# Kernel tuning notes

Hardware: AMD Instinct MI355X
Metric: run time of the kernel (lower is better)

Reference implementation:

```python
import math
import jax, jax.numpy as jnp
import numpy as np

DIM = 1024
NUM_HEADS = 16
HEAD_DIM = DIM // NUM_HEADS


def setup_inputs() -> dict:
    key = jax.random.key(0)
    ks = jax.random.split(key, 5)
    b, t, d = 2, 2048, DIM
    x = jax.random.normal(ks[0], (b, t, d), dtype=jnp.float32)
    mask = jnp.ones((b, t), dtype=jnp.float32)  # 1 = keep, 0 = pad
    s_in = 1.0 / math.sqrt(d)
    w_qkv = jax.random.normal(ks[1], (3 * d, d), dtype=jnp.float32) * s_in
    b_qkv = jnp.zeros((3 * d,), dtype=jnp.float32)
    w_out = jax.random.normal(ks[2], (d, d), dtype=jnp.float32) * s_in
    b_out = jnp.zeros((d,), dtype=jnp.float32)
    return {"x": x, "mask": mask, "w_qkv": w_qkv, "b_qkv": b_qkv,
            "w_out": w_out, "b_out": b_out}


def reference(x, mask, w_qkv, b_qkv, w_out, b_out):
    b, t, d = x.shape
    h, hd = NUM_HEADS, HEAD_DIM
    # qkv projection (torch Linear: x @ W^T + b)
    qkv = x @ w_qkv.T + b_qkv                          # [b,t,3d]
    q, k, v = jnp.split(qkv, 3, axis=-1)
    def reshape(z):
        return z.reshape(b, t, h, hd).transpose(0, 2, 1, 3)  # [b,h,t,hd]
    q, k, v = reshape(q), reshape(k), reshape(v)
    att = jnp.einsum('bhqd,bhkd->bhqk', q, k) / math.sqrt(hd)  # [b,h,t,t]
    causal = jnp.tril(jnp.ones((t, t), dtype=bool))            # [t,t]
    keep = causal[None, None, :, :] & (mask[:, None, None, :] != 0)
    att = jnp.where(keep, att, -jnp.inf)
    att = jax.nn.softmax(att, axis=-1)
    out = jnp.einsum('bhqk,bhkd->bhqd', att, v)        # [b,h,t,hd]
    out = out.transpose(0, 2, 1, 3).reshape(b, t, d)
    return out @ w_out.T + b_out
```

## Files before the change

kernel.cpp:

```cpp
#include <hip/hip_runtime.h>
#include <cmath>

#define B_ 2
#define T_ 2048
#define D_ 1024
#define H_ 16
#define HD_ 64
#define M_ (B_ * T_)
#define N3_ (3 * D_)
#define K_ 1024

typedef _Float16 halfx8 __attribute__((ext_vector_type(8)));
typedef _Float16 halfx4 __attribute__((ext_vector_type(4)));
typedef _Float16 halfx2 __attribute__((ext_vector_type(2)));
typedef __fp16 fp16x2 __attribute__((ext_vector_type(2)));
typedef float f32x4 __attribute__((ext_vector_type(4)));
typedef float f32x16 __attribute__((ext_vector_type(16)));

#define ASYNC_COPY16(gp, lp) \
  __builtin_amdgcn_global_load_lds((__attribute__((address_space(1))) void*)(gp), \
      (__attribute__((address_space(3))) void*)(lp), 16, 0, 0)

#define QSCALE 0.1803368801111204f
#define RTHR 4.0f

__device__ __forceinline__ float exp2fast(float x) {
#if __has_builtin(__builtin_amdgcn_exp2f)
    return __builtin_amdgcn_exp2f(x);
#else
    return exp2f(x);
#endif
}

__device__ const int QT2_OF[24] = {15,15,7, 14,14, 13,13,6, 12,12, 11,11,5, 10,10, 9,9,4, 8,8, 3,2,1,0};
__device__ const int C2_OF[24]  = { 0, 1,0,  0, 1,  0, 1,0,  0, 1,  0, 1,0,  0, 1, 0,1,0,  0,1, 0,0,0,0};

__global__ __launch_bounds__(256) void prep_all(
    const float* __restrict__ x, const float* __restrict__ wq,
    const float* __restrict__ wo, const float* __restrict__ mask,
    _Float16* __restrict__ xh, _Float16* __restrict__ wqh,
    _Float16* __restrict__ woh, float* __restrict__ kbias,
    int* __restrict__ tflags)
{
    int bid = blockIdx.x;
    if (bid >= 4096) {
        int i = (bid - 4096) * 256 + threadIdx.x;
        float mv = mask[i];
        kbias[i] = (mv != 0.f) ? 0.f : -INFINITY;
        unsigned long long bal = __ballot(mv != 0.f);
        if ((threadIdx.x & 63) == 0) tflags[i >> 6] = (bal == ~0ULL) ? 1 : 0;
        return;
    }
    const float* s; _Float16* d; int off;
    if (bid < 2048)      { s = x;  d = xh;  off = bid; }
    else if (bid < 3584) { s = wq; d = wqh; off = bid - 2048; }
    else                 { s = wo; d = woh; off = bid - 3584; }
    int i = (off * 256 + threadIdx.x) * 8;
    float4 a = *(const float4*)(s + i);
    float4 b = *(const float4*)(s + i + 4);
    halfx8 h;
    h[0] = (_Float16)a.x; h[1] = (_Float16)a.y; h[2] = (_Float16)a.z; h[3] = (_Float16)a.w;
    h[4] = (_Float16)b.x; h[5] = (_Float16)b.y; h[6] = (_Float16)b.z; h[7] = (_Float16)b.w;
    *(halfx8*)(d + i) = h;
}

__global__ __launch_bounds__(256) void gemm_qkv(
    const _Float16* __restrict__ A, const _Float16* __restrict__ Wt,
    const float* __restrict__ bias,
    _Float16* __restrict__ qh, _Float16* __restrict__ kh, _Float16* __restrict__ vth)
{
    __shared__ _Float16 As[128 * 32];
    __shared__ _Float16 Bs[128 * 32];
    const int tid = threadIdx.x;
    const int lane = tid & 63, w = tid >> 6;
    const int col = lane & 15, quad = lane >> 4;
    const int wr = w >> 1, wc = w & 1;
    const int m0 = blockIdx.y << 7, n0 = blockIdx.x << 7;

    const int c0 = w * 2, c1 = c0 + 1;
    const int r0 = c0 * 16 + (lane >> 2), r1 = c1 * 16 + (lane >> 2);
    const int ks = (lane & 3) << 3;

    f32x4 acc[4][4] = {};

    for (int k0 = 0; k0 < K_; k0 += 32) {
        ASYNC_COPY16(A  + (size_t)(m0 + r0) * K_ + k0 + ks, &As[c0 * 512]);
        ASYNC_COPY16(A  + (size_t)(m0 + r1) * K_ + k0 + ks, &As[c1 * 512]);
        ASYNC_COPY16(Wt + (size_t)(n0 + r0) * K_ + k0 + ks, &Bs[c0 * 512]);
        ASYNC_COPY16(Wt + (size_t)(n0 + r1) * K_ + k0 + ks, &Bs[c1 * 512]);
        __syncthreads();
        halfx8 af[4], bf[4];
#pragma unroll
        for (int i = 0; i < 4; ++i)
            af[i] = *(const halfx8*)&As[(wr * 64 + i * 16 + col) * 32 + quad * 8];
#pragma unroll
        for (int j = 0; j < 4; ++j)
            bf[j] = *(const halfx8*)&Bs[(wc * 64 + j * 16 + col) * 32 + quad * 8];
#pragma unroll
        for (int i = 0; i < 4; ++i)
#pragma unroll
            for (int j = 0; j < 4; ++j)
                acc[i][j] = __builtin_amdgcn_mfma_f32_16x16x32_f16(af[i], bf[j], acc[i][j], 0, 0, 0);
        __syncthreads();
    }

#pragma unroll
    for (int i = 0; i < 4; ++i) {
#pragma unroll
        for (int r = 0; r < 4; ++r) {
            int m = m0 + wr * 64 + i * 16 + quad * 4 + r;
            int bb = m >> 11, tt = m & (T_ - 1);
#pragma unroll
            for (int j = 0; j < 4; ++j) {
                int n = n0 + wc * 64 + j * 16 + col;
                float val = acc[i][j][r] + bias[n];
                int which = n >> 10, head = (n >> 6) & 15, dd = n & 63;
                if (which == 0) {
                    qh[((size_t)(bb * H_ + head) * T_ + tt) * HD_ + dd] = (_Float16)(val * QSCALE);
                } else if (which == 1) {
                    int hi = ((dd >> 3) ^ (tt & 7) ^ ((tt >> 3) & 7)) & 7;
                    int dds = (hi << 3) | (dd & 7);
                    kh[((size_t)(bb * H_ + head) * T_ + tt) * HD_ + dds] = (_Float16)val;
                } else {
                    int hi = (((tt >> 3) & 7) ^ (dd & 7) ^ ((dd >> 3) & 7)) & 7;
                    int tts = (tt & ~63) | (hi << 3) | (tt & 7);
                    vth[((size_t)(bb * H_ + head) * HD_ + dd) * T_ + tts] = (_Float16)val;
                }
            }
        }
    }
}

__global__ __launch_bounds__(256) void gemm_out(
    const _Float16* __restrict__ A, const _Float16* __restrict__ Wt,
    const float* __restrict__ bias, float* __restrict__ C)
{
    __shared__ _Float16 As[128 * 32];
    __shared__ _Float16 Bs[64 * 32];
    const int tid = threadIdx.x;
    const int lane = tid & 63, w = tid >> 6;
    const int col = lane & 15, quad = lane >> 4;
    const int m0 = blockIdx.y << 7, n0 = blockIdx.x << 6;

    const int c0 = w * 2, c1 = c0 + 1;
    const int rA0 = c0 * 16 + (lane >> 2), rA1 = c1 * 16 + (lane >> 2);
    const int rB = w * 16 + (lane >> 2);
    const int ks = (lane & 3) << 3;

    f32x4 acc[2][4] = {};

    for (int k0 = 0; k0 < K_; k0 += 32) {
        ASYNC_COPY16(A  + (size_t)(m0 + rA0) * K_ + k0 + ks, &As[c0 * 512]);
        ASYNC_COPY16(A  + (size_t)(m0 + rA1) * K_ + k0 + ks, &As[c1 * 512]);
        ASYNC_COPY16(Wt + (size_t)(n0 + rB) * K_ + k0 + ks, &Bs[w * 512]);
        __syncthreads();
        halfx8 af[2], bf[4];
#pragma unroll
        for (int i = 0; i < 2; ++i)
            af[i] = *(const halfx8*)&As[(w * 32 + i * 16 + col) * 32 + quad * 8];
#pragma unroll
        for (int j = 0; j < 4; ++j)
            bf[j] = *(const halfx8*)&Bs[(j * 16 + col) * 32 + quad * 8];
#pragma unroll
        for (int i = 0; i < 2; ++i)
#pragma unroll
            for (int j = 0; j < 4; ++j)
                acc[i][j] = __builtin_amdgcn_mfma_f32_16x16x32_f16(af[i], bf[j], acc[i][j], 0, 0, 0);
        __syncthreads();
    }

#pragma unroll
    for (int i = 0; i < 2; ++i) {
#pragma unroll
        for (int r = 0; r < 4; ++r) {
            int m = m0 + w * 32 + i * 16 + quad * 4 + r;
#pragma unroll
            for (int j = 0; j < 4; ++j) {
                int n = n0 + j * 16 + col;
                C[(size_t)m * D_ + n] = acc[i][j][r] + bias[n];
            }
        }
    }
}

__global__ __launch_bounds__(256, 3) void attn_kernel(
    const _Float16* __restrict__ qh, const _Float16* __restrict__ kh,
    const _Float16* __restrict__ vth, const float* __restrict__ kbias,
    const int* __restrict__ tflags,
    float* __restrict__ pm, float* __restrict__ pl,
    _Float16* __restrict__ po, _Float16* __restrict__ oh)
{
    __shared__ _Float16 Ks[2][64 * 64];
    __shared__ _Float16 Vt[2][64 * 64];

    const int item = blockIdx.x >> 5;
    const int qt = QT2_OF[item], c = C2_OF[item];
    const int hb = blockIdx.x & 31;
    const int h = hb & 15, b = hb >> 4;
    const bool split = (qt >= 8);
    const int tid = threadIdx.x;
    const int lane = tid & 63, w = tid >> 6;
    const int l31 = lane & 31, q2 = lane >> 5;

    const int kt0 = (split && c) ? (qt + 1) : 0;
    const int ktend = (split && !c) ? qt : (2 * qt + 1);

    const int bh = b * H_ + h;
    const _Float16* qp = qh + (size_t)bh * T_ * HD_;
    const _Float16* kp = kh + (size_t)bh * T_ * HD_;
    const _Float16* vp = vth + (size_t)bh * HD_ * T_;
    const float* kb = kbias + (size_t)b * T_;
    const int* tf = tflags + b * 32;

    const int qbase = qt * 128 + w * 32;
    const int q_row = qbase + l31;

    halfx8 bq[4];
#pragma unroll
    for (int hc = 0; hc < 4; ++hc)
        bq[hc] = *(const halfx8*)(qp + (size_t)q_row * HD_ + hc * 16 + q2 * 8);

    float mrow = -INFINITY;
    float lrow = 0.f;
    f32x16 oacc[2] = {};
    const fp16x2 one2 = {(__fp16)1.f, (__fp16)1.f};

    {
        const _Float16* ksrc = kp + (size_t)(kt0 * 64 + w * 16) * HD_;
        ASYNC_COPY16(ksrc + lane * 8, &Ks[0][(w * 16) * 64]);
        ASYNC_COPY16(ksrc + 8 * HD_ + lane * 8, &Ks[0][(w * 16 + 8) * 64]);
        const _Float16* vsrc = vp + (size_t)(w * 16 + (lane >> 3)) * T_
                                 + kt0 * 64 + (lane & 7) * 8;
        ASYNC_COPY16(vsrc, &Vt[0][(w * 16) * 64]);
        ASYNC_COPY16(vsrc + 8 * T_, &Vt[0][(w * 16 + 8) * 64]);
    }

    for (int kt = kt0; kt <= ktend; ++kt) {
        const int cur = (kt - kt0) & 1;
        __syncthreads();
        if (kt < ktend) {
            const int nb = cur ^ 1;
            const _Float16* ksrc = kp + (size_t)((kt + 1) * 64 + w * 16) * HD_;
            ASYNC_COPY16(ksrc + lane * 8, &Ks[nb][(w * 16) * 64]);
            ASYNC_COPY16(ksrc + 8 * HD_ + lane * 8, &Ks[nb][(w * 16 + 8) * 64]);
            const _Float16* vsrc = vp + (size_t)(w * 16 + (lane >> 3)) * T_
                                     + (kt + 1) * 64 + (lane & 7) * 8;
            ASYNC_COPY16(vsrc, &Vt[nb][(w * 16) * 64]);
            ASYNC_COPY16(vsrc + 8 * T_, &Vt[nb][(w * 16 + 8) * 64]);
        }
        if (kt * 64 > qbase + 31) continue;

        const int allkeep = tf[kt];
        const int kb2max = (qbase + 31 - kt * 64 >= 32) ? 2 : 1;

        auto qk_half = [&](int kb2v) -> f32x16 {
            f32x16 a = {};
#pragma unroll
            for (int hc = 0; hc < 4; ++hc) {
                int seg = (hc * 2 + q2) ^ (l31 & 7) ^ ((kb2v * 4 + (l31 >> 3)) & 7);
                halfx8 ka = *(const halfx8*)&Ks[cur][(kb2v * 32 + l31) * 64 + seg * 8];
                a = __builtin_amdgcn_mfma_f32_32x32x16_f16(ka, bq[hc], a, 0, 0, 0);
            }
            return a;
        };
        f32x16 sa0, sa1;
        __builtin_amdgcn_s_setprio(1);
        sa0 = qk_half(0);
        if (kb2max == 2) sa1 = qk_half(1);
        __builtin_amdgcn_s_setprio(0);

        auto smpv = [&](const f32x16& a, int kb2v) {
            float t0 = fmaxf(fmaxf(a[0],  a[1]),  a[2]);
            float t1 = fmaxf(fmaxf(a[3],  a[4]),  a[5]);
            float t2 = fmaxf(fmaxf(a[6],  a[7]),  a[8]);
            float t3 = fmaxf(fmaxf(a[9],  a[10]), a[11]);
            float t4 = fmaxf(fmaxf(a[12], a[13]), a[14]);
            float u0 = fmaxf(fmaxf(t0, t1), t2);
            float u1 = fmaxf(fmaxf(t3, t4), a[15]);
            float mx = fmaxf(u0, u1);

            if (__any(mx > mrow + RTHR)) {
                float mxo = fmaxf(mx, __shfl_xor(mx, 32, 64));
                float mnew = fmaxf(mrow, mxo);
                float alpha = exp2fast(mrow - mnew);
                lrow *= alpha;
#pragma unroll
                for (int db = 0; db < 2; ++db)
#pragma unroll
                    for (int r = 0; r < 16; ++r) oacc[db][r] *= alpha;
                mrow = mnew;
            }

            const bool fastk = allkeep && (kt * 64 + kb2v * 32 + 31 <= qbase);
            halfx4 pf[4];
            float s0 = 0.f, s1 = 0.f;
            if (fastk) {
#pragma unroll
                for (int cc = 0; cc < 4; ++cc) {
                    float e0 = exp2fast(a[cc * 4 + 0] - mrow);
                    float e1 = exp2fast(a[cc * 4 + 1] - mrow);
                    float e2 = exp2fast(a[cc * 4 + 2] - mrow);
                    float e3 = exp2fast(a[cc * 4 + 3] - mrow);
                    fp16x2 lo = __builtin_amdgcn_cvt_pkrtz(e0, e1);
                    fp16x2 hi = __builtin_amdgcn_cvt_pkrtz(e2, e3);
                    halfx2* pfv = (halfx2*)&pf[cc];
                    pfv[0] = __builtin_bit_cast(halfx2, lo);
                    pfv[1] = __builtin_bit_cast(halfx2, hi);
#if __has_builtin(__builtin_amdgcn_fdot2)
                    s0 = __builtin_amdgcn_fdot2(lo, one2, s0, false);
                    s1 = __builtin_amdgcn_fdot2(hi, one2, s1, false);
#else
                    s0 += e0 + e1; s1 += e2 + e3;
#endif
                }
            } else {
#pragma unroll
                for (int cc = 0; cc < 4; ++cc) {
                    float e[4];
#pragma unroll
                    for (int j = 0; j < 4; ++j) {
                        int key = kt * 64 + kb2v * 32 + 8 * cc + 4 * q2 + j;
                        float add = allkeep ? 0.f : kb[key];
                        e[j] = (key <= q_row) ? exp2fast(a[cc * 4 + j] + add - mrow) : 0.f;
                    }
                    fp16x2 lo = __builtin_amdgcn_cvt_pkrtz(e[0], e[1]);
                    fp16x2 hi = __builtin_amdgcn_cvt_pkrtz(e[2], e[3]);
                    halfx2* pfv = (halfx2*)&pf[cc];
                    pfv[0] = __builtin_bit_cast(halfx2, lo);
                    pfv[1] = __builtin_bit_cast(halfx2, hi);
#if __has_builtin(__builtin_amdgcn_fdot2)
                    s0 = __builtin_amdgcn_fdot2(lo, one2, s0, false);
                    s1 = __builtin_amdgcn_fdot2(hi, one2, s1, false);
#else
                    s0 += e[0] + e[1]; s1 += e[2] + e[3];
#endif
                }
            }
            lrow += s0 + s1;

            __builtin_amdgcn_s_setprio(1);
#pragma unroll
            for (int db = 0; db < 2; ++db)
#pragma unroll
                for (int cc = 0; cc < 4; ++cc) {
                    int ck = kb2v * 4 + cc;
                    int seg = ck ^ (l31 & 7) ^ ((db * 4 + (l31 >> 3)) & 7);
                    halfx4 va = *(const halfx4*)&Vt[cur][(db * 32 + l31) * 64 + seg * 8 + q2 * 4];
                    oacc[db] = __builtin_amdgcn_mfma_f32_32x32x8f16(va, pf[cc], oacc[db], 0, 0, 0);
                }
            __builtin_amdgcn_s_setprio(0);
        };

        smpv(sa0, 0);
        if (kb2max == 2) smpv(sa1, 1);
    }

    lrow += __shfl_xor(lrow, 32, 64);

    const int qloc = w * 32 + l31;
    _Float16* ohrow = oh + ((size_t)(b * T_ + qt * 128 + qloc)) * D_ + h * 64;

    if (!split) {
        const float linv = 1.f / lrow;
#pragma unroll
        for (int db = 0; db < 2; ++db)
#pragma unroll
            for (int gg = 0; gg < 4; ++gg) {
                halfx4 ov;
#pragma unroll
                for (int j = 0; j < 4; ++j)
                    ov[j] = (_Float16)(oacc[db][gg * 4 + j] * linv);
                *(halfx4*)(ohrow + db * 32 + 8 * gg + 4 * q2) = ov;
            }
    } else {
        const int slot = (bh * 8 + (qt - 8)) * 2 + c;
        if (q2 == 0) {
            pm[(size_t)slot * 128 + qloc] = mrow;
            pl[(size_t)slot * 128 + qloc] = lrow;
        }
        _Float16* pob = (c == 0) ? ohrow
                      : po + ((size_t)(bh * 8 + (qt - 8)) * 128 + qloc) * 64;
#pragma unroll
        for (int db = 0; db < 2; ++db)
#pragma unroll
            for (int gg = 0; gg < 4; ++gg) {
                halfx4 ov;
#pragma unroll
                for (int j = 0; j < 4; ++j)
                    ov[j] = (_Float16)(oacc[db][gg * 4 + j]);
                *(halfx4*)(pob + db * 32 + 8 * gg + 4 * q2) = ov;
            }
    }
}

__global__ __launch_bounds__(256) void attn_combine(
    const float* __restrict__ pm, const float* __restrict__ pl,
    const _Float16* __restrict__ po, _Float16* __restrict__ oh)
{
    const int qi = blockIdx.x;
    const int h = blockIdx.y, b = blockIdx.z;
    const int bh = b * H_ + h;
    const int tid = threadIdx.x;
    const int r = tid >> 1, dh = tid & 1;

    const int s0 = (bh * 8 + qi) * 2;
    float m0 = pm[(size_t)s0 * 128 + r],       m1 = pm[(size_t)(s0 + 1) * 128 + r];
    float l0 = pl[(size_t)s0 * 128 + r],       l1 = pl[(size_t)(s0 + 1) * 128 + r];
    float ms = fmaxf(m0, m1);
    float w0 = exp2f(m0 - ms), w1 = exp2f(m1 - ms);
    float linv = 1.f / (w0 * l0 + w1 * l1);
    w0 *= linv; w1 *= linv;

    _Float16* ohrow = oh + ((size_t)(b * T_ + (qi + 8) * 128 + r)) * D_ + h * 64 + dh * 32;
    const _Float16* src = po + ((size_t)(bh * 8 + qi) * 128 + r) * 64 + dh * 32;

#pragma unroll
    for (int g = 0; g < 4; ++g) {
        halfx8 o0 = *(const halfx8*)(ohrow + g * 8);
        halfx8 o1 = *(const halfx8*)(src + g * 8);
        halfx8 ov;
#pragma unroll
        for (int j = 0; j < 8; ++j)
            ov[j] = (_Float16)(w0 * (float)o0[j] + w1 * (float)o1[j]);
        *(halfx8*)(ohrow + g * 8) = ov;
    }
}

extern "C" void kernel_launch(void* const* d_in, const int* in_sizes, int n_in,
                              void* d_out, int out_size, void* d_ws, size_t ws_size,
                              hipStream_t stream)
{
    (void)in_sizes; (void)n_in; (void)out_size; (void)ws_size;
    const float* x     = (const float*)d_in[0];
    const float* mask  = (const float*)d_in[1];
    const float* w_qkv = (const float*)d_in[2];
    const float* b_qkv = (const float*)d_in[3];
    const float* w_out = (const float*)d_in[4];
    const float* b_out = (const float*)d_in[5];
    float* out = (float*)d_out;

    const size_t QKV1 = (size_t)B_ * H_ * T_ * HD_;
    _Float16* xh  = (_Float16*)d_ws;
    _Float16* wqh = xh  + (size_t)M_ * K_;
    _Float16* woh = wqh + (size_t)N3_ * K_;
    _Float16* qh  = woh + (size_t)D_ * K_;
    _Float16* kh  = qh  + QKV1;
    _Float16* vth = kh  + QKV1;
    _Float16* oh  = vth + QKV1;
    _Float16* po  = oh  + QKV1;
    float* kbias  = (float*)(po + (size_t)32 * 8 * 128 * 64);
    float* pm     = kbias + (size_t)B_ * T_;
    float* pl     = pm + (size_t)32 * 16 * 128;
    int* tflags   = (int*)(pl + (size_t)32 * 16 * 128);

    prep_all<<<4112, 256, 0, stream>>>(x, w_qkv, w_out, mask,
                                       xh, wqh, woh, kbias, tflags);
    gemm_qkv<<<dim3(N3_ / 128, M_ / 128), 256, 0, stream>>>(
        xh, wqh, b_qkv, qh, kh, vth);
    attn_kernel<<<dim3(768, 1, 1), 256, 0, stream>>>(
        qh, kh, vth, kbias, tflags, pm, pl, po, oh);
    attn_combine<<<dim3(8, H_, B_), 256, 0, stream>>>(
        pm, pl, po, oh);
    gemm_out<<<dim3(D_ / 64, M_ / 128), 256, 0, stream>>>(
        oh, woh, b_out, out);
}
```

Before: 181.7 us.

## Double-buffer LDS tiles in QKV and output GEMMs to overlap loads with MFMA

Result: slower. 189.2 us (+4.2%).

```diff
diff --git a/kernel.cpp b/kernel.cpp
--- a/kernel.cpp
+++ b/kernel.cpp
@@ -69,8 +69,8 @@
     const float* __restrict__ bias,
     _Float16* __restrict__ qh, _Float16* __restrict__ kh, _Float16* __restrict__ vth)
 {
-    __shared__ _Float16 As[128 * 32];
-    __shared__ _Float16 Bs[128 * 32];
+    __shared__ _Float16 As[2][128 * 32];
+    __shared__ _Float16 Bs[2][128 * 32];
     const int tid = threadIdx.x;
     const int lane = tid & 63, w = tid >> 6;
     const int col = lane & 15, quad = lane >> 4;
@@ -81,27 +81,41 @@
     const int r0 = c0 * 16 + (lane >> 2), r1 = c1 * 16 + (lane >> 2);
     const int ks = (lane & 3) << 3;
 
+    const _Float16* pA0 = A  + (size_t)(m0 + r0) * K_ + ks;
+    const _Float16* pA1 = A  + (size_t)(m0 + r1) * K_ + ks;
+    const _Float16* pB0 = Wt + (size_t)(n0 + r0) * K_ + ks;
+    const _Float16* pB1 = Wt + (size_t)(n0 + r1) * K_ + ks;
+
     f32x4 acc[4][4] = {};
 
-    for (int k0 = 0; k0 < K_; k0 += 32) {
-        ASYNC_COPY16(A  + (size_t)(m0 + r0) * K_ + k0 + ks, &As[c0 * 512]);
-        ASYNC_COPY16(A  + (size_t)(m0 + r1) * K_ + k0 + ks, &As[c1 * 512]);
-        ASYNC_COPY16(Wt + (size_t)(n0 + r0) * K_ + k0 + ks, &Bs[c0 * 512]);
-        ASYNC_COPY16(Wt + (size_t)(n0 + r1) * K_ + k0 + ks, &Bs[c1 * 512]);
+    ASYNC_COPY16(pA0, &As[0][c0 * 512]);
+    ASYNC_COPY16(pA1, &As[0][c1 * 512]);
+    ASYNC_COPY16(pB0, &Bs[0][c0 * 512]);
+    ASYNC_COPY16(pB1, &Bs[0][c1 * 512]);
+
+    for (int t = 0; t < 32; ++t) {
+        const int cur = t & 1;
         __syncthreads();
+        if (t < 31) {
+            const int nb = cur ^ 1;
+            pA0 += 32; pA1 += 32; pB0 += 32; pB1 += 32;
+            ASYNC_COPY16(pA0, &As[nb][c0 * 512]);
+            ASYNC_COPY16(pA1, &As[nb][c1 * 512]);
+            ASYNC_COPY16(pB0, &Bs[nb][c0 * 512]);
+            ASYNC_COPY16(pB1, &Bs[nb][c1 * 512]);
+        }
         halfx8 af[4], bf[4];
 #pragma unroll
         for (int i = 0; i < 4; ++i)
-            af[i] = *(const halfx8*)&As[(wr * 64 + i * 16 + col) * 32 + quad * 8];
+            af[i] = *(const halfx8*)&As[cur][(wr * 64 + i * 16 + col) * 32 + quad * 8];
 #pragma unroll
         for (int j = 0; j < 4; ++j)
-            bf[j] = *(const halfx8*)&Bs[(wc * 64 + j * 16 + col) * 32 + quad * 8];
+            bf[j] = *(const halfx8*)&Bs[cur][(wc * 64 + j * 16 + col) * 32 + quad * 8];
 #pragma unroll
         for (int i = 0; i < 4; ++i)
 #pragma unroll
             for (int j = 0; j < 4; ++j)
                 acc[i][j] = __builtin_amdgcn_mfma_f32_16x16x32_f16(af[i], bf[j], acc[i][j], 0, 0, 0);
-        __syncthreads();
     }
 
 #pragma unroll
@@ -135,8 +149,8 @@
     const _Float16* __restrict__ A, const _Float16* __restrict__ Wt,
     const float* __restrict__ bias, float* __restrict__ C)
 {
-    __shared__ _Float16 As[128 * 32];
-    __shared__ _Float16 Bs[64 * 32];
+    __shared__ _Float16 As[2][128 * 32];
+    __shared__ _Float16 Bs[2][64 * 32];
     const int tid = threadIdx.x;
     const int lane = tid & 63, w = tid >> 6;
     const int col = lane & 15, quad = lane >> 4;
@@ -147,26 +161,38 @@
     const int rB = w * 16 + (lane >> 2);
     const int ks = (lane & 3) << 3;
 
+    const _Float16* pA0 = A  + (size_t)(m0 + rA0) * K_ + ks;
+    const _Float16* pA1 = A  + (size_t)(m0 + rA1) * K_ + ks;
+    const _Float16* pB  = Wt + (size_t)(n0 + rB) * K_ + ks;
+
     f32x4 acc[2][4] = {};
 
-    for (int k0 = 0; k0 < K_; k0 += 32) {
-        ASYNC_COPY16(A  + (size_t)(m0 + rA0) * K_ + k0 + ks, &As[c0 * 512]);
-        ASYNC_COPY16(A  + (size_t)(m0 + rA1) * K_ + k0 + ks, &As[c1 * 512]);
-        ASYNC_COPY16(Wt + (size_t)(n0 + rB) * K_ + k0 + ks, &Bs[w * 512]);
+    ASYNC_COPY16(pA0, &As[0][c0 * 512]);
+    ASYNC_COPY16(pA1, &As[0][c1 * 512]);
+    ASYNC_COPY16(pB,  &Bs[0][w * 512]);
+
+    for (int t = 0; t < 32; ++t) {
+        const int cur = t & 1;
         __syncthreads();
+        if (t < 31) {
+            const int nb = cur ^ 1;
+            pA0 += 32; pA1 += 32; pB += 32;
+            ASYNC_COPY16(pA0, &As[nb][c0 * 512]);
+            ASYNC_COPY16(pA1, &As[nb][c1 * 512]);
+            ASYNC_COPY16(pB,  &Bs[nb][w * 512]);
+        }
         halfx8 af[2], bf[4];
 #pragma unroll
         for (int i = 0; i < 2; ++i)
-            af[i] = *(const halfx8*)&As[(w * 32 + i * 16 + col) * 32 + quad * 8];
+            af[i] = *(const halfx8*)&As[cur][(w * 32 + i * 16 + col) * 32 + quad * 8];
 #pragma unroll
         for (int j = 0; j < 4; ++j)
-            bf[j] = *(const halfx8*)&Bs[(j * 16 + col) * 32 + quad * 8];
+            bf[j] = *(const halfx8*)&Bs[cur][(j * 16 + col) * 32 + quad * 8];
 #pragma unroll
         for (int i = 0; i < 2; ++i)
 #pragma unroll
             for (int j = 0; j < 4; ++j)
                 acc[i][j] = __builtin_amdgcn_mfma_f32_16x16x32_f16(af[i], bf[j], acc[i][j], 0, 0, 0);
-        __syncthreads();
     }
 
 #pragma unroll
```
